# Optimization experiments

Measured on AMD Instinct MI355X. Metric: run time of the kernel, lower is better.

## Reference

```python
import jax, jax.numpy as jnp
import numpy as np

N_NODES = 50000
N_EDGES = 800000
D = 128
NEG_SLOPE = 0.01
LN_EPS = 1e-5


def gcn_conv(x, W, b, src, dst, n_nodes):
    # Linear transform: [N, D_in] @ [D_in, D_out]
    h = x @ W
    # Symmetric degree normalization (self-loops already included in src/dst)
    deg = jax.ops.segment_sum(jnp.ones_like(dst, dtype=h.dtype), dst, num_segments=n_nodes)
    dinv = jnp.where(deg > 0, jax.lax.rsqrt(deg), 0.0)
    coef = dinv[src] * dinv[dst]                      # [E]
    msg = h[src] * coef[:, None]                      # gather + scale, [E, D]
    out = jax.ops.segment_sum(msg, dst, num_segments=n_nodes)  # scatter-add
    return out + b


def layer_norm(x, gamma, beta):
    mu = jnp.mean(x, axis=-1, keepdims=True)
    var = jnp.mean(jnp.square(x - mu), axis=-1, keepdims=True)
    return (x - mu) * jax.lax.rsqrt(var + LN_EPS) * gamma + beta


def setup_inputs() -> dict:
    key = jax.random.key(0)
    ks = jax.random.split(key, 8)
    x = jax.random.normal(ks[0], (N_NODES, D), dtype=jnp.float32)
    edge_index = jax.random.randint(ks[1], (2, N_EDGES), 0, N_NODES, dtype=jnp.int64)
    s = 1.0 / np.sqrt(D)
    W1 = jax.random.uniform(ks[2], (D, D), jnp.float32, -s, s)
    b1 = jnp.zeros((D,), jnp.float32)
    W2 = jax.random.uniform(ks[3], (D, D), jnp.float32, -s, s)
    b2 = jnp.zeros((D,), jnp.float32)
    ln1_g = jnp.ones((D,), jnp.float32)
    ln1_b = jnp.zeros((D,), jnp.float32)
    ln2_g = jnp.ones((D,), jnp.float32)
    ln2_b = jnp.zeros((D,), jnp.float32)
    return {"x": x, "edge_index": edge_index, "W1": W1, "b1": b1,
            "ln1_g": ln1_g, "ln1_b": ln1_b, "W2": W2, "b2": b2,
            "ln2_g": ln2_g, "ln2_b": ln2_b}


def reference(x, edge_index, W1, b1, ln1_g, ln1_b, W2, b2, ln2_g, ln2_b):
    n = x.shape[0]
    # add self-loops (PyG GCNConv default)
    loops = jnp.arange(n, dtype=edge_index.dtype)
    src = jnp.concatenate([edge_index[0], loops])
    dst = jnp.concatenate([edge_index[1], loops])

    residual = x
    h = gcn_conv(x, W1, b1, src, dst, n)
    h = jax.nn.leaky_relu(h, NEG_SLOPE)
    h = layer_norm(h + residual, ln1_g, ln1_b)
    h = gcn_conv(h, W2, b2, src, dst, n)
    return jax.nn.leaky_relu(layer_norm(h + residual, ln2_g, ln2_b), NEG_SLOPE)
```

## Files before the change

kernel.cpp:

```cpp
#include <hip/hip_runtime.h>
#include <hip/hip_bf16.h>

#define NN 50000
#define NE 800000
#define D 128
#define NEG_SLOPE 0.01f
#define LN_EPS 1e-5f

#define NPB 256
#define NB 196
#define CAP 6144
#define ECH 8192
#define NCH ((NE + ECH - 1) / ECH)

typedef __attribute__((ext_vector_type(8))) short bf16x8;
typedef __attribute__((ext_vector_type(4))) float f32x4;
typedef __attribute__((ext_vector_type(4))) int i32x4;

__device__ inline unsigned short f2bf(float f) {
    unsigned u = __float_as_uint(f);
    unsigned r = 0x7FFFu + ((u >> 16) & 1u);
    return (unsigned short)((u + r) >> 16);
}
__device__ inline void bf2x(unsigned u, float& lo, float& hi) {
    lo = __uint_as_float(u << 16);
    hi = __uint_as_float(u & 0xFFFF0000u);
}


__global__ __launch_bounds__(256) void bucket_scatter(const int* __restrict__ src,
                                                      const int* __restrict__ dst,
                                                      int* __restrict__ bcursor,
                                                      int2* __restrict__ bedge) {
    __shared__ int hist[NB], lcur[NB], gbase[NB];
    int t = threadIdx.x;
    int e0 = blockIdx.x * ECH;
    int ecnt = min(ECH, NE - e0);
    if (t < NB) hist[t] = 0;
    __syncthreads();
    for (int k = t; k < ecnt; k += 256) atomicAdd(&hist[dst[e0 + k] >> 8], 1);
    __syncthreads();
    if (t < NB) {
        gbase[t] = atomicAdd(&bcursor[t], hist[t]);
        lcur[t] = 0;
    }
    __syncthreads();
    for (int k = t; k < ecnt; k += 256) {
        int s = src[e0 + k], d = dst[e0 + k];
        int b = d >> 8;
        int p = atomicAdd(&lcur[b], 1);
        bedge[(size_t)b * CAP + gbase[b] + p] = make_int2(s, d);
    }
}

__global__ __launch_bounds__(256) void node_count(const int2* __restrict__ bedge,
                                                  const int* __restrict__ bcnt,
                                                  float* __restrict__ dinv,
                                                  int2* __restrict__ rowinfo,
                                                  int* __restrict__ ticket) {
    __shared__ int h[NPB];
    __shared__ int tmp[256];
    __shared__ int base;
    int b = blockIdx.x, t = threadIdx.x;
    h[t] = 0;
    __syncthreads();
    int s0 = b * CAP, s1 = s0 + bcnt[b];
    for (int k = s0 + t; k < s1; k += 256) atomicAdd(&h[bedge[k].y & 255], 1);
    __syncthreads();
    int deg = h[t];
    int node = b * NPB + t;
    int pdeg = (deg + 7) & ~7;
    tmp[t] = pdeg;
    __syncthreads();
    for (int off = 1; off < 256; off <<= 1) {
        int uu = (t >= off) ? tmp[t - off] : 0;
        __syncthreads();
        tmp[t] += uu;
        __syncthreads();
    }
    if (t == 255) base = atomicAdd(ticket, tmp[255]);
    __syncthreads();
    if (node < NN) {
        dinv[node] = rsqrtf((float)(deg + 1));
        rowinfo[node] = make_int2(base + tmp[t] - pdeg, pdeg);
    }
}

__global__ __launch_bounds__(256) void csr_scatter(const int2* __restrict__ bedge,
                                                   const int* __restrict__ bcnt,
                                                   const int2* __restrict__ rowinfo,
                                                   const float* __restrict__ dinv,
                                                   int2* __restrict__ csr_pair) {
    __shared__ int cur[NPB];
    __shared__ int rl[NPB];
    __shared__ float sdinv[NPB];
    int b = blockIdx.x, t = threadIdx.x;
    int node = b * NPB + t;
    rl[t] = (node < NN) ? rowinfo[node].x : 0;
    sdinv[t] = (node < NN) ? dinv[node] : 0.f;
    cur[t] = 0;
    __syncthreads();
    int s0 = b * CAP, s1 = s0 + bcnt[b];
    for (int k = s0 + t; k < s1; k += 256) {
        int2 eg = bedge[k];
        int li = eg.y & 255;
        int p = atomicAdd(&cur[li], 1);
        float coef = dinv[eg.x] * sdinv[li];
        csr_pair[rl[li] + p] = make_int2(eg.x, __float_as_int(coef));
    }
    __syncthreads();
    int dgc = cur[t];
    int pend = (dgc + 7) & ~7;
    int selfsrc = (node < NN) ? node : 0;
    for (int k = dgc; k < pend; ++k)
        csr_pair[rl[t] + k] = make_int2(selfsrc, 0);
}

__global__ void wt_pack2(const float* __restrict__ W1, const float* __restrict__ W2,
                         unsigned short* __restrict__ WT1, unsigned short* __restrict__ WT2) {
    int tid = blockIdx.x * 256 + threadIdx.x;
    const float* W = (tid < D * D) ? W1 : W2;
    unsigned short* WT = (tid < D * D) ? WT1 : WT2;
    int id = tid & (D * D - 1);
    int nn = id & 127, k = id >> 7;
    WT[nn * 128 + k] = f2bf(W[k * 128 + nn]);
}

__global__ __launch_bounds__(256) void gemm_mfma(const float* __restrict__ A,
                                                 const unsigned short* __restrict__ WT,
                                                 unsigned short* __restrict__ out, int n) {
    __shared__ __align__(16) unsigned short a_lds[64 * 128];
    __shared__ __align__(16) unsigned short w_lds[128 * 128];
    int t = threadIdx.x;
    int m0 = blockIdx.x * 64;

    #pragma unroll
    for (int it = 0; it < 8; ++it) {
        int idx = it * 256 + t;
        int row = idx >> 4, c = idx & 15;
        uint4 v = *(const uint4*)&WT[row * 128 + c * 8];
        int byte = (row * 256 + c * 16) ^ ((row & 7) << 4);
        *(uint4*)((char*)w_lds + byte) = v;
    }
    #pragma unroll
    for (int it = 0; it < 4; ++it) {
        int idx = it * 256 + t;
        int row = idx >> 4, c = idx & 15;
        int grow = m0 + row;
        uint4 w = make_uint4(0u, 0u, 0u, 0u);
        if (grow < n) {
            float4 v0 = *(const float4*)&A[(size_t)grow * D + c * 8];
            float4 v1 = *(const float4*)&A[(size_t)grow * D + c * 8 + 4];
            w.x = (unsigned)f2bf(v0.x) | ((unsigned)f2bf(v0.y) << 16);
            w.y = (unsigned)f2bf(v0.z) | ((unsigned)f2bf(v0.w) << 16);
            w.z = (unsigned)f2bf(v1.x) | ((unsigned)f2bf(v1.y) << 16);
            w.w = (unsigned)f2bf(v1.z) | ((unsigned)f2bf(v1.w) << 16);
        }
        int byte = (row * 256 + c * 16) ^ ((row & 7) << 4);
        *(uint4*)((char*)a_lds + byte) = w;
    }
    __syncthreads();

    int wv = t >> 6, l = t & 63;
    int lrow = l & 15, lgrp = l >> 4;
    int arow = wv * 16 + lrow;

    f32x4 acc[8];
    #pragma unroll
    for (int nf = 0; nf < 8; ++nf) acc[nf] = (f32x4){0.f, 0.f, 0.f, 0.f};

    #pragma unroll
    for (int kk = 0; kk < 4; ++kk) {
        int abyte = (arow * 256 + kk * 64 + lgrp * 16) ^ ((arow & 7) << 4);
        bf16x8 afrag = *(bf16x8*)((char*)a_lds + abyte);
        #pragma unroll
        for (int nf = 0; nf < 8; ++nf) {
            int bcol = nf * 16 + lrow;
            int bbyte = (bcol * 256 + kk * 64 + lgrp * 16) ^ ((bcol & 7) << 4);
            bf16x8 bfrag = *(bf16x8*)((char*)w_lds + bbyte);
            acc[nf] = __builtin_amdgcn_mfma_f32_16x16x32_bf16(afrag, bfrag, acc[nf], 0, 0, 0);
        }
    }

    #pragma unroll
    for (int nf = 0; nf < 8; ++nf) {
        #pragma unroll
        for (int r = 0; r < 4; ++r) {
            int grow = m0 + wv * 16 + lgrp * 4 + r;
            if (grow < n) out[(size_t)grow * D + nf * 16 + lrow] = f2bf(acc[nf][r]);
        }
    }
}


__device__ inline void agg8(const unsigned* __restrict__ h, const int2* __restrict__ csr_pair,
                            int e, int lane, float& accx, float& accy) {
    i32x4 q0 = __builtin_nontemporal_load((const i32x4*)(csr_pair + e + 0));
    i32x4 q1 = __builtin_nontemporal_load((const i32x4*)(csr_pair + e + 2));
    i32x4 q2 = __builtin_nontemporal_load((const i32x4*)(csr_pair + e + 4));
    i32x4 q3 = __builtin_nontemporal_load((const i32x4*)(csr_pair + e + 6));
    unsigned g0 = h[(size_t)q0[0] * (D / 2) + lane];
    unsigned g1 = h[(size_t)q0[2] * (D / 2) + lane];
    unsigned g2 = h[(size_t)q1[0] * (D / 2) + lane];
    unsigned g3 = h[(size_t)q1[2] * (D / 2) + lane];
    unsigned g4 = h[(size_t)q2[0] * (D / 2) + lane];
    unsigned g5 = h[(size_t)q2[2] * (D / 2) + lane];
    unsigned g6 = h[(size_t)q3[0] * (D / 2) + lane];
    unsigned g7 = h[(size_t)q3[2] * (D / 2) + lane];
    float ax, ay, c;
    c = __int_as_float(q0[1]); bf2x(g0, ax, ay); accx = fmaf(c, ax, accx); accy = fmaf(c, ay, accy);
    c = __int_as_float(q0[3]); bf2x(g1, ax, ay); accx = fmaf(c, ax, accx); accy = fmaf(c, ay, accy);
    c = __int_as_float(q1[1]); bf2x(g2, ax, ay); accx = fmaf(c, ax, accx); accy = fmaf(c, ay, accy);
    c = __int_as_float(q1[3]); bf2x(g3, ax, ay); accx = fmaf(c, ax, accx); accy = fmaf(c, ay, accy);
    c = __int_as_float(q2[1]); bf2x(g4, ax, ay); accx = fmaf(c, ax, accx); accy = fmaf(c, ay, accy);
    c = __int_as_float(q2[3]); bf2x(g5, ax, ay); accx = fmaf(c, ax, accx); accy = fmaf(c, ay, accy);
    c = __int_as_float(q3[1]); bf2x(g6, ax, ay); accx = fmaf(c, ax, accx); accy = fmaf(c, ay, accy);
    c = __int_as_float(q3[3]); bf2x(g7, ax, ay); accx = fmaf(c, ax, accx); accy = fmaf(c, ay, accy);
}

__device__ inline void agg_2node(const unsigned* __restrict__ h,
                                 const int2* __restrict__ csr_pair,
                                 int eA, int eA1, int eB, int eB1, int lane,
                                 float& aAx, float& aAy, float& aBx, float& aBy) {
    while (eA < eA1 && eB < eB1) {
        i32x4 qA0 = __builtin_nontemporal_load((const i32x4*)(csr_pair + eA + 0));
        i32x4 qA1 = __builtin_nontemporal_load((const i32x4*)(csr_pair + eA + 2));
        i32x4 qA2 = __builtin_nontemporal_load((const i32x4*)(csr_pair + eA + 4));
        i32x4 qA3 = __builtin_nontemporal_load((const i32x4*)(csr_pair + eA + 6));
        i32x4 qB0 = __builtin_nontemporal_load((const i32x4*)(csr_pair + eB + 0));
        i32x4 qB1 = __builtin_nontemporal_load((const i32x4*)(csr_pair + eB + 2));
        i32x4 qB2 = __builtin_nontemporal_load((const i32x4*)(csr_pair + eB + 4));
        i32x4 qB3 = __builtin_nontemporal_load((const i32x4*)(csr_pair + eB + 6));
        unsigned gA0 = h[(size_t)qA0[0] * (D / 2) + lane];
        unsigned gA1 = h[(size_t)qA0[2] * (D / 2) + lane];
        unsigned gA2 = h[(size_t)qA1[0] * (D / 2) + lane];
        unsigned gA3 = h[(size_t)qA1[2] * (D / 2) + lane];
        unsigned gA4 = h[(size_t)qA2[0] * (D / 2) + lane];
        unsigned gA5 = h[(size_t)qA2[2] * (D / 2) + lane];
        unsigned gA6 = h[(size_t)qA3[0] * (D / 2) + lane];
        unsigned gA7 = h[(size_t)qA3[2] * (D / 2) + lane];
        unsigned gB0 = h[(size_t)qB0[0] * (D / 2) + lane];
        unsigned gB1 = h[(size_t)qB0[2] * (D / 2) + lane];
        unsigned gB2 = h[(size_t)qB1[0] * (D / 2) + lane];
        unsigned gB3 = h[(size_t)qB1[2] * (D / 2) + lane];
        unsigned gB4 = h[(size_t)qB2[0] * (D / 2) + lane];
        unsigned gB5 = h[(size_t)qB2[2] * (D / 2) + lane];
        unsigned gB6 = h[(size_t)qB3[0] * (D / 2) + lane];
        unsigned gB7 = h[(size_t)qB3[2] * (D / 2) + lane];
        float ax, ay, c;
        c = __int_as_float(qA0[1]); bf2x(gA0, ax, ay); aAx = fmaf(c, ax, aAx); aAy = fmaf(c, ay, aAy);
        c = __int_as_float(qA0[3]); bf2x(gA1, ax, ay); aAx = fmaf(c, ax, aAx); aAy = fmaf(c, ay, aAy);
        c = __int_as_float(qA1[1]); bf2x(gA2, ax, ay); aAx = fmaf(c, ax, aAx); aAy = fmaf(c, ay, aAy);
        c = __int_as_float(qA1[3]); bf2x(gA3, ax, ay); aAx = fmaf(c, ax, aAx); aAy = fmaf(c, ay, aAy);
        c = __int_as_float(qA2[1]); bf2x(gA4, ax, ay); aAx = fmaf(c, ax, aAx); aAy = fmaf(c, ay, aAy);
        c = __int_as_float(qA2[3]); bf2x(gA5, ax, ay); aAx = fmaf(c, ax, aAx); aAy = fmaf(c, ay, aAy);
        c = __int_as_float(qA3[1]); bf2x(gA6, ax, ay); aAx = fmaf(c, ax, aAx); aAy = fmaf(c, ay, aAy);
        c = __int_as_float(qA3[3]); bf2x(gA7, ax, ay); aAx = fmaf(c, ax, aAx); aAy = fmaf(c, ay, aAy);
        c = __int_as_float(qB0[1]); bf2x(gB0, ax, ay); aBx = fmaf(c, ax, aBx); aBy = fmaf(c, ay, aBy);
        c = __int_as_float(qB0[3]); bf2x(gB1, ax, ay); aBx = fmaf(c, ax, aBx); aBy = fmaf(c, ay, aBy);
        c = __int_as_float(qB1[1]); bf2x(gB2, ax, ay); aBx = fmaf(c, ax, aBx); aBy = fmaf(c, ay, aBy);
        c = __int_as_float(qB1[3]); bf2x(gB3, ax, ay); aBx = fmaf(c, ax, aBx); aBy = fmaf(c, ay, aBy);
        c = __int_as_float(qB2[1]); bf2x(gB4, ax, ay); aBx = fmaf(c, ax, aBx); aBy = fmaf(c, ay, aBy);
        c = __int_as_float(qB2[3]); bf2x(gB5, ax, ay); aBx = fmaf(c, ax, aBx); aBy = fmaf(c, ay, aBy);
        c = __int_as_float(qB3[1]); bf2x(gB6, ax, ay); aBx = fmaf(c, ax, aBx); aBy = fmaf(c, ay, aBy);
        c = __int_as_float(qB3[3]); bf2x(gB7, ax, ay); aBx = fmaf(c, ax, aBx); aBy = fmaf(c, ay, aBy);
        eA += 8; eB += 8;
    }
    while (eA < eA1) { agg8(h, csr_pair, eA, lane, aAx, aAy); eA += 8; }
    while (eB < eB1) { agg8(h, csr_pair, eB, lane, aBx, aBy); eB += 8; }
}

__global__ __launch_bounds__(512) void agg_ln1_gemm(const unsigned* __restrict__ h,
                                                    const float* __restrict__ x,
                                                    const float* __restrict__ bias,
                                                    const float* __restrict__ gamma,
                                                    const float* __restrict__ beta,
                                                    const float* __restrict__ dinv,
                                                    const int2* __restrict__ rowinfo,
                                                    const int2* __restrict__ csr_pair,
                                                    const unsigned short* __restrict__ wt2,
                                                    unsigned short* __restrict__ hbf2) {
    __shared__ __align__(16) unsigned short w_lds[128 * 128];
    __shared__ __align__(16) unsigned short a_lds[16 * 128];
    int t = threadIdx.x;

    #pragma unroll
    for (int it = 0; it < 4; ++it) {
        int idx = it * 512 + t;
        int row = idx >> 4, c = idx & 15;
        uint4 v = *(const uint4*)&wt2[row * 128 + c * 8];
        int byte = (row * 256 + c * 16) ^ ((row & 7) << 4);
        *(uint4*)((char*)w_lds + byte) = v;
    }

    int wid = t >> 6, lane = t & 63;
    int iA = blockIdx.x * 16 + wid * 2;
    int iB = iA + 1;
    float diA = dinv[iA], diB = dinv[iB];

    float hx, hy;
    bf2x(h[(size_t)iA * (D / 2) + lane], hx, hy);
    float aAx = diA * diA * hx, aAy = diA * diA * hy;
    bf2x(h[(size_t)iB * (D / 2) + lane], hx, hy);
    float aBx = diB * diB * hx, aBy = diB * diB * hy;

    int2 riA = rowinfo[iA];
    int2 riB = rowinfo[iB];
    int eA = __builtin_amdgcn_readfirstlane(riA.x);
    int eA1 = eA + __builtin_amdgcn_readfirstlane(riA.y);
    int eB = __builtin_amdgcn_readfirstlane(riB.x);
    int eB1 = eB + __builtin_amdgcn_readfirstlane(riB.y);
    agg_2node(h, csr_pair, eA, eA1, eB, eB1, lane, aAx, aAy, aBx, aBy);

    float2 bv = *(const float2*)&bias[2 * lane];
    float2 gv = *(const float2*)&gamma[2 * lane];
    float2 bt = *(const float2*)&beta[2 * lane];

    aAx += bv.x; aAy += bv.y;
    aBx += bv.x; aBy += bv.y;
    aAx = aAx > 0.f ? aAx : NEG_SLOPE * aAx;
    aAy = aAy > 0.f ? aAy : NEG_SLOPE * aAy;
    aBx = aBx > 0.f ? aBx : NEG_SLOPE * aBx;
    aBy = aBy > 0.f ? aBy : NEG_SLOPE * aBy;

    size_t rowA = (size_t)iA * D + 2 * lane;
    size_t rowB = (size_t)iB * D + 2 * lane;
    float2 xA = *(const float2*)&x[rowA];
    float2 xB = *(const float2*)&x[rowB];
    float vA0 = aAx + xA.x, vA1 = aAy + xA.y;
    float vB0 = aBx + xB.x, vB1 = aBy + xB.y;

    float sA1 = vA0 + vA1, sA2 = vA0 * vA0 + vA1 * vA1;
    float sB1 = vB0 + vB1, sB2 = vB0 * vB0 + vB1 * vB1;
    #pragma unroll
    for (int off = 1; off < 64; off <<= 1) {
        sA1 += __shfl_xor(sA1, off, 64);
        sA2 += __shfl_xor(sA2, off, 64);
        sB1 += __shfl_xor(sB1, off, 64);
        sB2 += __shfl_xor(sB2, off, 64);
    }
    float muA = sA1 * (1.f / 128.f);
    float varA = fmaxf(sA2 * (1.f / 128.f) - muA * muA, 0.f);
    float rsA = rsqrtf(varA + LN_EPS);
    float muB = sB1 * (1.f / 128.f);
    float varB = fmaxf(sB2 * (1.f / 128.f) - muB * muB, 0.f);
    float rsB = rsqrtf(varB + LN_EPS);

    float oA0 = (vA0 - muA) * rsA * gv.x + bt.x;
    float oA1 = (vA1 - muA) * rsA * gv.y + bt.y;
    float oB0 = (vB0 - muB) * rsB * gv.x + bt.x;
    float oB1 = (vB1 - muB) * rsB * gv.y + bt.y;

    int rA = wid * 2, rB = wid * 2 + 1;
    unsigned dwA = (unsigned)f2bf(oA0) | ((unsigned)f2bf(oA1) << 16);
    unsigned dwB = (unsigned)f2bf(oB0) | ((unsigned)f2bf(oB1) << 16);
    int byteA = (rA * 256 + lane * 4) ^ ((rA & 7) << 4);
    int byteB = (rB * 256 + lane * 4) ^ ((rB & 7) << 4);
    *(unsigned*)((char*)a_lds + byteA) = dwA;
    *(unsigned*)((char*)a_lds + byteB) = dwB;
    __syncthreads();

    int lrow = lane & 15, lgrp = lane >> 4;
    f32x4 acc = (f32x4){0.f, 0.f, 0.f, 0.f};
    #pragma unroll
    for (int kk = 0; kk < 4; ++kk) {
        int abyte = (lrow * 256 + kk * 64 + lgrp * 16) ^ ((lrow & 7) << 4);
        bf16x8 afrag = *(bf16x8*)((char*)a_lds + abyte);
        int bcol = wid * 16 + lrow;
        int bbyte = (bcol * 256 + kk * 64 + lgrp * 16) ^ ((bcol & 7) << 4);
        bf16x8 bfrag = *(bf16x8*)((char*)w_lds + bbyte);
        acc = __builtin_amdgcn_mfma_f32_16x16x32_bf16(afrag, bfrag, acc, 0, 0, 0);
    }
    #pragma unroll
    for (int r = 0; r < 4; ++r) {
        int grow = blockIdx.x * 16 + lgrp * 4 + r;
        hbf2[(size_t)grow * D + wid * 16 + lrow] = f2bf(acc[r]);
    }
}

__global__ __launch_bounds__(256) void agg_ln2(const unsigned* __restrict__ h,
                                               const float* __restrict__ x,
                                               const float* __restrict__ bias,
                                               const float* __restrict__ gamma,
                                               const float* __restrict__ beta,
                                               const float* __restrict__ dinv,
                                               const int2* __restrict__ rowinfo,
                                               const int2* __restrict__ csr_pair,
                                               float* __restrict__ out) {
    int wid = threadIdx.x >> 6;
    int lane = threadIdx.x & 63;
    int iA = blockIdx.x * 8 + wid * 2;
    int iB = iA + 1;
    float diA = dinv[iA], diB = dinv[iB];

    float hx, hy;
    bf2x(h[(size_t)iA * (D / 2) + lane], hx, hy);
    float aAx = diA * diA * hx, aAy = diA * diA * hy;
    bf2x(h[(size_t)iB * (D / 2) + lane], hx, hy);
    float aBx = diB * diB * hx, aBy = diB * diB * hy;

    int2 riA = rowinfo[iA];
    int2 riB = rowinfo[iB];
    int eA = __builtin_amdgcn_readfirstlane(riA.x);
    int eA1 = eA + __builtin_amdgcn_readfirstlane(riA.y);
    int eB = __builtin_amdgcn_readfirstlane(riB.x);
    int eB1 = eB + __builtin_amdgcn_readfirstlane(riB.y);
    agg_2node(h, csr_pair, eA, eA1, eB, eB1, lane, aAx, aAy, aBx, aBy);

    float2 bv = *(const float2*)&bias[2 * lane];
    float2 gv = *(const float2*)&gamma[2 * lane];
    float2 bt = *(const float2*)&beta[2 * lane];

    aAx += bv.x; aAy += bv.y;
    aBx += bv.x; aBy += bv.y;
    size_t rowA = (size_t)iA * D + 2 * lane;
    size_t rowB = (size_t)iB * D + 2 * lane;
    float2 xA = *(const float2*)&x[rowA];
    float2 xB = *(const float2*)&x[rowB];
    float vA0 = aAx + xA.x, vA1 = aAy + xA.y;
    float vB0 = aBx + xB.x, vB1 = aBy + xB.y;

    float sA1 = vA0 + vA1, sA2 = vA0 * vA0 + vA1 * vA1;
    float sB1 = vB0 + vB1, sB2 = vB0 * vB0 + vB1 * vB1;
    #pragma unroll
    for (int off = 1; off < 64; off <<= 1) {
        sA1 += __shfl_xor(sA1, off, 64);
        sA2 += __shfl_xor(sA2, off, 64);
        sB1 += __shfl_xor(sB1, off, 64);
        sB2 += __shfl_xor(sB2, off, 64);
    }
    float muA = sA1 * (1.f / 128.f);
    float varA = fmaxf(sA2 * (1.f / 128.f) - muA * muA, 0.f);
    float rsA = rsqrtf(varA + LN_EPS);
    float muB = sB1 * (1.f / 128.f);
    float varB = fmaxf(sB2 * (1.f / 128.f) - muB * muB, 0.f);
    float rsB = rsqrtf(varB + LN_EPS);

    float oA0 = (vA0 - muA) * rsA * gv.x + bt.x;
    float oA1 = (vA1 - muA) * rsA * gv.y + bt.y;
    float oB0 = (vB0 - muB) * rsB * gv.x + bt.x;
    float oB1 = (vB1 - muB) * rsB * gv.y + bt.y;
    oA0 = oA0 > 0.f ? oA0 : NEG_SLOPE * oA0;
    oA1 = oA1 > 0.f ? oA1 : NEG_SLOPE * oA1;
    oB0 = oB0 > 0.f ? oB0 : NEG_SLOPE * oB0;
    oB1 = oB1 > 0.f ? oB1 : NEG_SLOPE * oB1;
    *(float2*)&out[rowA] = make_float2(oA0, oA1);
    *(float2*)&out[rowB] = make_float2(oB0, oB1);
}

extern "C" void kernel_launch(void* const* d_in, const int* in_sizes, int n_in,
                              void* d_out, int out_size, void* d_ws, size_t ws_size,
                              hipStream_t stream) {
    const float* x    = (const float*)d_in[0];
    const int*   ei   = (const int*)d_in[1];
    const float* W1   = (const float*)d_in[2];
    const float* b1   = (const float*)d_in[3];
    const float* ln1g = (const float*)d_in[4];
    const float* ln1b = (const float*)d_in[5];
    const float* W2   = (const float*)d_in[6];
    const float* b2   = (const float*)d_in[7];
    const float* ln2g = (const float*)d_in[8];
    const float* ln2b = (const float*)d_in[9];
    float* out = (float*)d_out;

    const int* srcp = ei;
    const int* dstp = ei + NE;

    char* ws = (char*)d_ws;
    size_t p = 0;
    auto alloc = [&](size_t bytes) {
        char* r = ws + p;
        p += (bytes + 255) & ~(size_t)255;
        return r;
    };
    int*   bcursor  = (int*)alloc((NB + 1) * 4);
    int2*  rowinfo  = (int2*)alloc((size_t)NN * 8);
    float* dinv     = (float*)alloc(NN * 4);
    int2*  bedge    = (int2*)alloc((size_t)NB * CAP * 8);
    int2*  csr_pair = (int2*)alloc(((size_t)NE + 8 * NN) * 8);
    unsigned short* hbf  = (unsigned short*)alloc((size_t)NN * D * 2);
    unsigned short* hbf2 = (unsigned short*)alloc((size_t)NN * D * 2);
    unsigned short* wt1  = (unsigned short*)alloc(D * D * 2);
    unsigned short* wt2  = (unsigned short*)alloc(D * D * 2);

    hipMemsetAsync(bcursor, 0, (NB + 1) * 4, stream);

    wt_pack2<<<2 * D * D / 256, 256, 0, stream>>>(W1, W2, wt1, wt2);

    bucket_scatter<<<NCH, 256, 0, stream>>>(srcp, dstp, bcursor, bedge);
    gemm_mfma<<<(NN + 63) / 64, 256, 0, stream>>>(x, wt1, hbf, NN);
    node_count<<<NB, 256, 0, stream>>>(bedge, bcursor, dinv, rowinfo, &bcursor[NB]);
    csr_scatter<<<NB, 256, 0, stream>>>(bedge, bcursor, rowinfo, dinv, csr_pair);

    agg_ln1_gemm<<<NN / 16, 512, 0, stream>>>((const unsigned*)hbf, x, b1, ln1g, ln1b,
                                              dinv, rowinfo, csr_pair, wt2, hbf2);

    agg_ln2<<<NN / 8, 256, 0, stream>>>((const unsigned*)hbf2, x, b2, ln2g, ln2b,
                                        dinv, rowinfo, csr_pair, out);
}
```

Baseline: 133.7 us.

## Fold degree normalization into GEMM outputs and store source-only CSR

Splits the symmetric GCN coefficient: the source-side dinv now scales the GEMM output rows, and the destination-side dinv is applied once per node after aggregation. With no per-edge coefficient left, the CSR array holds only 4-byte source indices instead of 8-byte (src, coef) pairs, which halves index traffic in the gather loops and removes an FMA per edge. Padding entries point to an extra zeroed row (index NN) appended to each feature buffer. The dual-node gather loop is also widened to 16 edges per step to keep more loads in flight. The trade-offs are more register pressure and a reordered launch so the first GEMM waits for dinv.

```diff
diff --git a/kernel.cpp b/kernel.cpp
--- a/kernel.cpp
+++ b/kernel.cpp
@@ -89,15 +89,12 @@
 __global__ __launch_bounds__(256) void csr_scatter(const int2* __restrict__ bedge,
                                                    const int* __restrict__ bcnt,
                                                    const int2* __restrict__ rowinfo,
-                                                   const float* __restrict__ dinv,
-                                                   int2* __restrict__ csr_pair) {
+                                                   int* __restrict__ csr_src) {
     __shared__ int cur[NPB];
     __shared__ int rl[NPB];
-    __shared__ float sdinv[NPB];
     int b = blockIdx.x, t = threadIdx.x;
     int node = b * NPB + t;
     rl[t] = (node < NN) ? rowinfo[node].x : 0;
-    sdinv[t] = (node < NN) ? dinv[node] : 0.f;
     cur[t] = 0;
     __syncthreads();
     int s0 = b * CAP, s1 = s0 + bcnt[b];
@@ -105,20 +102,24 @@
         int2 eg = bedge[k];
         int li = eg.y & 255;
         int p = atomicAdd(&cur[li], 1);
-        float coef = dinv[eg.x] * sdinv[li];
-        csr_pair[rl[li] + p] = make_int2(eg.x, __float_as_int(coef));
+        csr_src[rl[li] + p] = eg.x;
     }
     __syncthreads();
     int dgc = cur[t];
     int pend = (dgc + 7) & ~7;
-    int selfsrc = (node < NN) ? node : 0;
     for (int k = dgc; k < pend; ++k)
-        csr_pair[rl[t] + k] = make_int2(selfsrc, 0);
+        csr_src[rl[t] + k] = NN;
 }
 
 __global__ void wt_pack2(const float* __restrict__ W1, const float* __restrict__ W2,
-                         unsigned short* __restrict__ WT1, unsigned short* __restrict__ WT2) {
+                         unsigned short* __restrict__ WT1, unsigned short* __restrict__ WT2,
+                         unsigned short* __restrict__ hbf, unsigned short* __restrict__ hbf2) {
     int tid = blockIdx.x * 256 + threadIdx.x;
+    if (tid < 32) {
+        uint4 z = make_uint4(0u, 0u, 0u, 0u);
+        if (tid < 16) *(uint4*)&hbf[(size_t)NN * D + tid * 8] = z;
+        else          *(uint4*)&hbf2[(size_t)NN * D + (tid - 16) * 8] = z;
+    }
     const float* W = (tid < D * D) ? W1 : W2;
     unsigned short* WT = (tid < D * D) ? WT1 : WT2;
     int id = tid & (D * D - 1);
@@ -128,6 +129,7 @@
 
 __global__ __launch_bounds__(256) void gemm_mfma(const float* __restrict__ A,
                                                  const unsigned short* __restrict__ WT,
+                                                 const float* __restrict__ dinv,
                                                  unsigned short* __restrict__ out, int n) {
     __shared__ __align__(16) unsigned short a_lds[64 * 128];
     __shared__ __align__(16) unsigned short w_lds[128 * 128];
@@ -183,91 +185,128 @@
     }
 
     #pragma unroll
-    for (int nf = 0; nf < 8; ++nf) {
-        #pragma unroll
-        for (int r = 0; r < 4; ++r) {
-            int grow = m0 + wv * 16 + lgrp * 4 + r;
-            if (grow < n) out[(size_t)grow * D + nf * 16 + lrow] = f2bf(acc[nf][r]);
+    for (int r = 0; r < 4; ++r) {
+        int grow = m0 + wv * 16 + lgrp * 4 + r;
+        if (grow < n) {
+            float dv = dinv[grow];
+            #pragma unroll
+            for (int nf = 0; nf < 8; ++nf)
+                out[(size_t)grow * D + nf * 16 + lrow] = f2bf(dv * acc[nf][r]);
         }
     }
 }
 
 
-__device__ inline void agg8(const unsigned* __restrict__ h, const int2* __restrict__ csr_pair,
-                            int e, int lane, float& accx, float& accy) {
-    i32x4 q0 = __builtin_nontemporal_load((const i32x4*)(csr_pair + e + 0));
-    i32x4 q1 = __builtin_nontemporal_load((const i32x4*)(csr_pair + e + 2));
-    i32x4 q2 = __builtin_nontemporal_load((const i32x4*)(csr_pair + e + 4));
-    i32x4 q3 = __builtin_nontemporal_load((const i32x4*)(csr_pair + e + 6));
-    unsigned g0 = h[(size_t)q0[0] * (D / 2) + lane];
-    unsigned g1 = h[(size_t)q0[2] * (D / 2) + lane];
-    unsigned g2 = h[(size_t)q1[0] * (D / 2) + lane];
-    unsigned g3 = h[(size_t)q1[2] * (D / 2) + lane];
-    unsigned g4 = h[(size_t)q2[0] * (D / 2) + lane];
-    unsigned g5 = h[(size_t)q2[2] * (D / 2) + lane];
-    unsigned g6 = h[(size_t)q3[0] * (D / 2) + lane];
-    unsigned g7 = h[(size_t)q3[2] * (D / 2) + lane];
-    float ax, ay, c;
-    c = __int_as_float(q0[1]); bf2x(g0, ax, ay); accx = fmaf(c, ax, accx); accy = fmaf(c, ay, accy);
-    c = __int_as_float(q0[3]); bf2x(g1, ax, ay); accx = fmaf(c, ax, accx); accy = fmaf(c, ay, accy);
-    c = __int_as_float(q1[1]); bf2x(g2, ax, ay); accx = fmaf(c, ax, accx); accy = fmaf(c, ay, accy);
-    c = __int_as_float(q1[3]); bf2x(g3, ax, ay); accx = fmaf(c, ax, accx); accy = fmaf(c, ay, accy);
-    c = __int_as_float(q2[1]); bf2x(g4, ax, ay); accx = fmaf(c, ax, accx); accy = fmaf(c, ay, accy);
-    c = __int_as_float(q2[3]); bf2x(g5, ax, ay); accx = fmaf(c, ax, accx); accy = fmaf(c, ay, accy);
-    c = __int_as_float(q3[1]); bf2x(g6, ax, ay); accx = fmaf(c, ax, accx); accy = fmaf(c, ay, accy);
-    c = __int_as_float(q3[3]); bf2x(g7, ax, ay); accx = fmaf(c, ax, accx); accy = fmaf(c, ay, accy);
+__device__ inline void agg8s(const unsigned* __restrict__ h, const int* __restrict__ csr,
+                             int e, int lane, float& ax_, float& ay_) {
+    i32x4 s0 = __builtin_nontemporal_load((const i32x4*)(csr + e));
+    i32x4 s1 = __builtin_nontemporal_load((const i32x4*)(csr + e + 4));
+    unsigned g0 = h[(size_t)s0[0] * (D / 2) + lane];
+    unsigned g1 = h[(size_t)s0[1] * (D / 2) + lane];
+    unsigned g2 = h[(size_t)s0[2] * (D / 2) + lane];
+    unsigned g3 = h[(size_t)s0[3] * (D / 2) + lane];
+    unsigned g4 = h[(size_t)s1[0] * (D / 2) + lane];
+    unsigned g5 = h[(size_t)s1[1] * (D / 2) + lane];
+    unsigned g6 = h[(size_t)s1[2] * (D / 2) + lane];
+    unsigned g7 = h[(size_t)s1[3] * (D / 2) + lane];
+    float lo, hi;
+    bf2x(g0, lo, hi); ax_ += lo; ay_ += hi;
+    bf2x(g1, lo, hi); ax_ += lo; ay_ += hi;
+    bf2x(g2, lo, hi); ax_ += lo; ay_ += hi;
+    bf2x(g3, lo, hi); ax_ += lo; ay_ += hi;
+    bf2x(g4, lo, hi); ax_ += lo; ay_ += hi;
+    bf2x(g5, lo, hi); ax_ += lo; ay_ += hi;
+    bf2x(g6, lo, hi); ax_ += lo; ay_ += hi;
+    bf2x(g7, lo, hi); ax_ += lo; ay_ += hi;
 }
 
 __device__ inline void agg_2node(const unsigned* __restrict__ h,
-                                 const int2* __restrict__ csr_pair,
+                                 const int* __restrict__ csr,
                                  int eA, int eA1, int eB, int eB1, int lane,
                                  float& aAx, float& aAy, float& aBx, float& aBy) {
-    while (eA < eA1 && eB < eB1) {
-        i32x4 qA0 = __builtin_nontemporal_load((const i32x4*)(csr_pair + eA + 0));
-        i32x4 qA1 = __builtin_nontemporal_load((const i32x4*)(csr_pair + eA + 2));
-        i32x4 qA2 = __builtin_nontemporal_load((const i32x4*)(csr_pair + eA + 4));
-        i32x4 qA3 = __builtin_nontemporal_load((const i32x4*)(csr_pair + eA + 6));
-        i32x4 qB0 = __builtin_nontemporal_load((const i32x4*)(csr_pair + eB + 0));
-        i32x4 qB1 = __builtin_nontemporal_load((const i32x4*)(csr_pair + eB + 2));
-        i32x4 qB2 = __builtin_nontemporal_load((const i32x4*)(csr_pair + eB + 4));
-        i32x4 qB3 = __builtin_nontemporal_load((const i32x4*)(csr_pair + eB + 6));
-        unsigned gA0 = h[(size_t)qA0[0] * (D / 2) + lane];
-        unsigned gA1 = h[(size_t)qA0[2] * (D / 2) + lane];
-        unsigned gA2 = h[(size_t)qA1[0] * (D / 2) + lane];
-        unsigned gA3 = h[(size_t)qA1[2] * (D / 2) + lane];
-        unsigned gA4 = h[(size_t)qA2[0] * (D / 2) + lane];
-        unsigned gA5 = h[(size_t)qA2[2] * (D / 2) + lane];
-        unsigned gA6 = h[(size_t)qA3[0] * (D / 2) + lane];
-        unsigned gA7 = h[(size_t)qA3[2] * (D / 2) + lane];
-        unsigned gB0 = h[(size_t)qB0[0] * (D / 2) + lane];
-        unsigned gB1 = h[(size_t)qB0[2] * (D / 2) + lane];
-        unsigned gB2 = h[(size_t)qB1[0] * (D / 2) + lane];
-        unsigned gB3 = h[(size_t)qB1[2] * (D / 2) + lane];
-        unsigned gB4 = h[(size_t)qB2[0] * (D / 2) + lane];
-        unsigned gB5 = h[(size_t)qB2[2] * (D / 2) + lane];
-        unsigned gB6 = h[(size_t)qB3[0] * (D / 2) + lane];
-        unsigned gB7 = h[(size_t)qB3[2] * (D / 2) + lane];
-        float ax, ay, c;
-        c = __int_as_float(qA0[1]); bf2x(gA0, ax, ay); aAx = fmaf(c, ax, aAx); aAy = fmaf(c, ay, aAy);
-        c = __int_as_float(qA0[3]); bf2x(gA1, ax, ay); aAx = fmaf(c, ax, aAx); aAy = fmaf(c, ay, aAy);
-        c = __int_as_float(qA1[1]); bf2x(gA2, ax, ay); aAx = fmaf(c, ax, aAx); aAy = fmaf(c, ay, aAy);
-        c = __int_as_float(qA1[3]); bf2x(gA3, ax, ay); aAx = fmaf(c, ax, aAx); aAy = fmaf(c, ay, aAy);
-        c = __int_as_float(qA2[1]); bf2x(gA4, ax, ay); aAx = fmaf(c, ax, aAx); aAy = fmaf(c, ay, aAy);
-        c = __int_as_float(qA2[3]); bf2x(gA5, ax, ay); aAx = fmaf(c, ax, aAx); aAy = fmaf(c, ay, aAy);
-        c = __int_as_float(qA3[1]); bf2x(gA6, ax, ay); aAx = fmaf(c, ax, aAx); aAy = fmaf(c, ay, aAy);
-        c = __int_as_float(qA3[3]); bf2x(gA7, ax, ay); aAx = fmaf(c, ax, aAx); aAy = fmaf(c, ay, aAy);
-        c = __int_as_float(qB0[1]); bf2x(gB0, ax, ay); aBx = fmaf(c, ax, aBx); aBy = fmaf(c, ay, aBy);
-        c = __int_as_float(qB0[3]); bf2x(gB1, ax, ay); aBx = fmaf(c, ax, aBx); aBy = fmaf(c, ay, aBy);
-        c = __int_as_float(qB1[1]); bf2x(gB2, ax, ay); aBx = fmaf(c, ax, aBx); aBy = fmaf(c, ay, aBy);
-        c = __int_as_float(qB1[3]); bf2x(gB3, ax, ay); aBx = fmaf(c, ax, aBx); aBy = fmaf(c, ay, aBy);
-        c = __int_as_float(qB2[1]); bf2x(gB4, ax, ay); aBx = fmaf(c, ax, aBx); aBy = fmaf(c, ay, aBy);
-        c = __int_as_float(qB2[3]); bf2x(gB5, ax, ay); aBx = fmaf(c, ax, aBx); aBy = fmaf(c, ay, aBy);
-        c = __int_as_float(qB3[1]); bf2x(gB6, ax, ay); aBx = fmaf(c, ax, aBx); aBy = fmaf(c, ay, aBy);
-        c = __int_as_float(qB3[3]); bf2x(gB7, ax, ay); aBx = fmaf(c, ax, aBx); aBy = fmaf(c, ay, aBy);
+    while (eA + 16 <= eA1 && eB + 16 <= eB1) {
+        i32x4 sA0 = __builtin_nontemporal_load((const i32x4*)(csr + eA));
+        i32x4 sA1 = __builtin_nontemporal_load((const i32x4*)(csr + eA + 4));
+        i32x4 sA2 = __builtin_nontemporal_load((const i32x4*)(csr + eA + 8));
+        i32x4 sA3 = __builtin_nontemporal_load((const i32x4*)(csr + eA + 12));
+        i32x4 sB0 = __builtin_nontemporal_load((const i32x4*)(csr + eB));
+        i32x4 sB1 = __builtin_nontemporal_load((const i32x4*)(csr + eB + 4));
+        i32x4 sB2 = __builtin_nontemporal_load((const i32x4*)(csr + eB + 8));
+        i32x4 sB3 = __builtin_nontemporal_load((const i32x4*)(csr + eB + 12));
+        unsigned gA0 = h[(size_t)sA0[0] * (D / 2) + lane];
+        unsigned gA1 = h[(size_t)sA0[1] * (D / 2) + lane];
+        unsigned gA2 = h[(size_t)sA0[2] * (D / 2) + lane];
+        unsigned gA3 = h[(size_t)sA0[3] * (D / 2) + lane];
+        unsigned gA4 = h[(size_t)sA1[0] * (D / 2) + lane];
+        unsigned gA5 = h[(size_t)sA1[1] * (D / 2) + lane];
+        unsigned gA6 = h[(size_t)sA1[2] * (D / 2) + lane];
+        unsigned gA7 = h[(size_t)sA1[3] * (D / 2) + lane];
+        unsigned gA8 = h[(size_t)sA2[0] * (D / 2) + lane];
+        unsigned gA9 = h[(size_t)sA2[1] * (D / 2) + lane];
+        unsigned gAa = h[(size_t)sA2[2] * (D / 2) + lane];
+        unsigned gAb = h[(size_t)sA2[3] * (D / 2) + lane];
+        unsigned gAc = h[(size_t)sA3[0] * (D / 2) + lane];
+        unsigned gAd = h[(size_t)sA3[1] * (D / 2) + lane];
+        unsigned gAe = h[(size_t)sA3[2] * (D / 2) + lane];
+        unsigned gAf = h[(size_t)sA3[3] * (D / 2) + lane];
+        unsigned gB0 = h[(size_t)sB0[0] * (D / 2) + lane];
+        unsigned gB1 = h[(size_t)sB0[1] * (D / 2) + lane];
+        unsigned gB2 = h[(size_t)sB0[2] * (D / 2) + lane];
+        unsigned gB3 = h[(size_t)sB0[3] * (D / 2) + lane];
+        unsigned gB4 = h[(size_t)sB1[0] * (D / 2) + lane];
+        unsigned gB5 = h[(size_t)sB1[1] * (D / 2) + lane];
+        unsigned gB6 = h[(size_t)sB1[2] * (D / 2) + lane];
+        unsigned gB7 = h[(size_t)sB1[3] * (D / 2) + lane];
+        unsigned gB8 = h[(size_t)sB2[0] * (D / 2) + lane];
+        unsigned gB9 = h[(size_t)sB2[1] * (D / 2) + lane];
+        unsigned gBa = h[(size_t)sB2[2] * (D / 2) + lane];
+        unsigned gBb = h[(size_t)sB2[3] * (D / 2) + lane];
+        unsigned gBc = h[(size_t)sB3[0] * (D / 2) + lane];
+        unsigned gBd = h[(size_t)sB3[1] * (D / 2) + lane];
+        unsigned gBe = h[(size_t)sB3[2] * (D / 2) + lane];
+        unsigned gBf = h[(size_t)sB3[3] * (D / 2) + lane];
+        float lo, hi;
+        bf2x(gA0, lo, hi); aAx += lo; aAy += hi;
+        bf2x(gA1, lo, hi); aAx += lo; aAy += hi;
+        bf2x(gA2, lo, hi); aAx += lo; aAy += hi;
+        bf2x(gA3, lo, hi); aAx += lo; aAy += hi;
+        bf2x(gA4, lo, hi); aAx += lo; aAy += hi;
+        bf2x(gA5, lo, hi); aAx += lo; aAy += hi;
+        bf2x(gA6, lo, hi); aAx += lo; aAy += hi;
+        bf2x(gA7, lo, hi); aAx += lo; aAy += hi;
+        bf2x(gA8, lo, hi); aAx += lo; aAy += hi;
+        bf2x(gA9, lo, hi); aAx += lo; aAy += hi;
+        bf2x(gAa, lo, hi); aAx += lo; aAy += hi;
+        bf2x(gAb, lo, hi); aAx += lo; aAy += hi;
+        bf2x(gAc, lo, hi); aAx += lo; aAy += hi;
+        bf2x(gAd, lo, hi); aAx += lo; aAy += hi;
+        bf2x(gAe, lo, hi); aAx += lo; aAy += hi;
+        bf2x(gAf, lo, hi); aAx += lo; aAy += hi;
+        bf2x(gB0, lo, hi); aBx += lo; aBy += hi;
+        bf2x(gB1, lo, hi); aBx += lo; aBy += hi;
+        bf2x(gB2, lo, hi); aBx += lo; aBy += hi;
+        bf2x(gB3, lo, hi); aBx += lo; aBy += hi;
+        bf2x(gB4, lo, hi); aBx += lo; aBy += hi;
+        bf2x(gB5, lo, hi); aBx += lo; aBy += hi;
+        bf2x(gB6, lo, hi); aBx += lo; aBy += hi;
+        bf2x(gB7, lo, hi); aBx += lo; aBy += hi;
+        bf2x(gB8, lo, hi); aBx += lo; aBy += hi;
+        bf2x(gB9, lo, hi); aBx += lo; aBy += hi;
+        bf2x(gBa, lo, hi); aBx += lo; aBy += hi;
+        bf2x(gBb, lo, hi); aBx += lo; aBy += hi;
+        bf2x(gBc, lo, hi); aBx += lo; aBy += hi;
+        bf2x(gBd, lo, hi); aBx += lo; aBy += hi;
+        bf2x(gBe, lo, hi); aBx += lo; aBy += hi;
+        bf2x(gBf, lo, hi); aBx += lo; aBy += hi;
+        eA += 16; eB += 16;
+    }
+    while (eA + 8 <= eA1 && eB + 8 <= eB1) {
+        agg8s(h, csr, eA, lane, aAx, aAy);
+        agg8s(h, csr, eB, lane, aBx, aBy);
         eA += 8; eB += 8;
     }
-    while (eA < eA1) { agg8(h, csr_pair, eA, lane, aAx, aAy); eA += 8; }
-    while (eB < eB1) { agg8(h, csr_pair, eB, lane, aBx, aBy); eB += 8; }
+    while (eA < eA1) { agg8s(h, csr, eA, lane, aAx, aAy); eA += 8; }
+    while (eB < eB1) { agg8s(h, csr, eB, lane, aBx, aBy); eB += 8; }
 }
 
 __global__ __launch_bounds__(512) void agg_ln1_gemm(const unsigned* __restrict__ h,
@@ -277,7 +316,7 @@
                                                     const float* __restrict__ beta,
                                                     const float* __restrict__ dinv,
                                                     const int2* __restrict__ rowinfo,
-                                                    const int2* __restrict__ csr_pair,
+                                                    const int* __restrict__ csr_src,
                                                     const unsigned short* __restrict__ wt2,
                                                     unsigned short* __restrict__ hbf2) {
     __shared__ __align__(16) unsigned short w_lds[128 * 128];
@@ -298,11 +337,9 @@
     int iB = iA + 1;
     float diA = dinv[iA], diB = dinv[iB];
 
-    float hx, hy;
-    bf2x(h[(size_t)iA * (D / 2) + lane], hx, hy);
-    float aAx = diA * diA * hx, aAy = diA * diA * hy;
-    bf2x(h[(size_t)iB * (D / 2) + lane], hx, hy);
-    float aBx = diB * diB * hx, aBy = diB * diB * hy;
+    float aAx, aAy, aBx, aBy;
+    bf2x(h[(size_t)iA * (D / 2) + lane], aAx, aAy);
+    bf2x(h[(size_t)iB * (D / 2) + lane], aBx, aBy);
 
     int2 riA = rowinfo[iA];
     int2 riB = rowinfo[iB];
@@ -310,14 +347,14 @@
     int eA1 = eA + __builtin_amdgcn_readfirstlane(riA.y);
     int eB = __builtin_amdgcn_readfirstlane(riB.x);
     int eB1 = eB + __builtin_amdgcn_readfirstlane(riB.y);
-    agg_2node(h, csr_pair, eA, eA1, eB, eB1, lane, aAx, aAy, aBx, aBy);
+    agg_2node(h, csr_src, eA, eA1, eB, eB1, lane, aAx, aAy, aBx, aBy);
 
     float2 bv = *(const float2*)&bias[2 * lane];
     float2 gv = *(const float2*)&gamma[2 * lane];
     float2 bt = *(const float2*)&beta[2 * lane];
 
-    aAx += bv.x; aAy += bv.y;
-    aBx += bv.x; aBy += bv.y;
+    aAx = fmaf(diA, aAx, bv.x); aAy = fmaf(diA, aAy, bv.y);
+    aBx = fmaf(diB, aBx, bv.x); aBy = fmaf(diB, aBy, bv.y);
     aAx = aAx > 0.f ? aAx : NEG_SLOPE * aAx;
     aAy = aAy > 0.f ? aAy : NEG_SLOPE * aAy;
     aBx = aBx > 0.f ? aBx : NEG_SLOPE * aBx;
@@ -374,7 +411,7 @@
     #pragma unroll
     for (int r = 0; r < 4; ++r) {
         int grow = blockIdx.x * 16 + lgrp * 4 + r;
-        hbf2[(size_t)grow * D + wid * 16 + lrow] = f2bf(acc[r]);
+        hbf2[(size_t)grow * D + wid * 16 + lrow] = f2bf(dinv[grow] * acc[r]);
     }
 }
 
@@ -385,7 +422,7 @@
                                                const float* __restrict__ beta,
                                                const float* __restrict__ dinv,
                                                const int2* __restrict__ rowinfo,
-                                               const int2* __restrict__ csr_pair,
+                                               const int* __restrict__ csr_src,
                                                float* __restrict__ out) {
     int wid = threadIdx.x >> 6;
     int lane = threadIdx.x & 63;
@@ -393,11 +430,9 @@
     int iB = iA + 1;
     float diA = dinv[iA], diB = dinv[iB];
 
-    float hx, hy;
-    bf2x(h[(size_t)iA * (D / 2) + lane], hx, hy);
-    float aAx = diA * diA * hx, aAy = diA * diA * hy;
-    bf2x(h[(size_t)iB * (D / 2) + lane], hx, hy);
-    float aBx = diB * diB * hx, aBy = diB * diB * hy;
+    float aAx, aAy, aBx, aBy;
+    bf2x(h[(size_t)iA * (D / 2) + lane], aAx, aAy);
+    bf2x(h[(size_t)iB * (D / 2) + lane], aBx, aBy);
 
     int2 riA = rowinfo[iA];
     int2 riB = rowinfo[iB];
@@ -405,14 +440,14 @@
     int eA1 = eA + __builtin_amdgcn_readfirstlane(riA.y);
     int eB = __builtin_amdgcn_readfirstlane(riB.x);
     int eB1 = eB + __builtin_amdgcn_readfirstlane(riB.y);
-    agg_2node(h, csr_pair, eA, eA1, eB, eB1, lane, aAx, aAy, aBx, aBy);
+    agg_2node(h, csr_src, eA, eA1, eB, eB1, lane, aAx, aAy, aBx, aBy);
 
     float2 bv = *(const float2*)&bias[2 * lane];
     float2 gv = *(const float2*)&gamma[2 * lane];
     float2 bt = *(const float2*)&beta[2 * lane];
 
-    aAx += bv.x; aAy += bv.y;
-    aBx += bv.x; aBy += bv.y;
+    aAx = fmaf(diA, aAx, bv.x); aAy = fmaf(diA, aAy, bv.y);
+    aBx = fmaf(diB, aBx, bv.x); aBy = fmaf(diB, aBy, bv.y);
     size_t rowA = (size_t)iA * D + 2 * lane;
     size_t rowB = (size_t)iB * D + 2 * lane;
     float2 xA = *(const float2*)&x[rowA];
@@ -477,24 +512,24 @@
     int2*  rowinfo  = (int2*)alloc((size_t)NN * 8);
     float* dinv     = (float*)alloc(NN * 4);
     int2*  bedge    = (int2*)alloc((size_t)NB * CAP * 8);
-    int2*  csr_pair = (int2*)alloc(((size_t)NE + 8 * NN) * 8);
-    unsigned short* hbf  = (unsigned short*)alloc((size_t)NN * D * 2);
-    unsigned short* hbf2 = (unsigned short*)alloc((size_t)NN * D * 2);
+    int*   csr_src  = (int*)alloc(((size_t)NE + 8 * NN) * 4);
+    unsigned short* hbf  = (unsigned short*)alloc((size_t)(NN + 8) * D * 2);
+    unsigned short* hbf2 = (unsigned short*)alloc((size_t)(NN + 8) * D * 2);
     unsigned short* wt1  = (unsigned short*)alloc(D * D * 2);
     unsigned short* wt2  = (unsigned short*)alloc(D * D * 2);
 
     hipMemsetAsync(bcursor, 0, (NB + 1) * 4, stream);
 
-    wt_pack2<<<2 * D * D / 256, 256, 0, stream>>>(W1, W2, wt1, wt2);
+    wt_pack2<<<2 * D * D / 256, 256, 0, stream>>>(W1, W2, wt1, wt2, hbf, hbf2);
 
     bucket_scatter<<<NCH, 256, 0, stream>>>(srcp, dstp, bcursor, bedge);
-    gemm_mfma<<<(NN + 63) / 64, 256, 0, stream>>>(x, wt1, hbf, NN);
     node_count<<<NB, 256, 0, stream>>>(bedge, bcursor, dinv, rowinfo, &bcursor[NB]);
-    csr_scatter<<<NB, 256, 0, stream>>>(bedge, bcursor, rowinfo, dinv, csr_pair);
+    gemm_mfma<<<(NN + 63) / 64, 256, 0, stream>>>(x, wt1, dinv, hbf, NN);
+    csr_scatter<<<NB, 256, 0, stream>>>(bedge, bcursor, rowinfo, csr_src);
 
     agg_ln1_gemm<<<NN / 16, 512, 0, stream>>>((const unsigned*)hbf, x, b1, ln1g, ln1b,
-                                              dinv, rowinfo, csr_pair, wt2, hbf2);
+                                              dinv, rowinfo, csr_src, wt2, hbf2);
 
     agg_ln2<<<NN / 8, 256, 0, stream>>>((const unsigned*)hbf2, x, b2, ln2g, ln2b,
-                                        dinv, rowinfo, csr_pair, out);
-}
+                                        dinv, rowinfo, csr_src, out);
+}
```

Result: faster. 130.1 us (-2.7%).
